# Optimization experiments

Hardware: AMD Instinct MI355X
Metric: run time of the kernel (lower is better)

The kernel has to match this reference:

```python
import jax, jax.numpy as jnp
import numpy as np

N, D_IN, H, D_EMB = 2048, 128, 256, 64


def setup_inputs() -> dict:
    key = jax.random.key(0)
    ks = jax.random.split(key, 8)
    x = jax.random.normal(ks[0], (N, D_IN), dtype=jnp.float32)
    adj = jnp.zeros((N, N), dtype=jnp.float32)  # only its last dim is used (eye sizing)
    s = 0.05
    W0 = jax.random.normal(ks[1], (D_IN, H), dtype=jnp.float32) * s
    b0 = jnp.zeros((H,), dtype=jnp.float32)
    W1 = jax.random.normal(ks[2], (H, D_EMB), dtype=jnp.float32) * s
    b1 = jnp.zeros((D_EMB,), dtype=jnp.float32)
    W2 = jax.random.normal(ks[3], (D_IN, D_IN), dtype=jnp.float32) * s
    b2 = jnp.zeros((D_IN,), dtype=jnp.float32)
    temp = jnp.float32(0.1)
    theta = jnp.float32(0.1)
    return {"x": x, "adj": adj, "W0": W0, "b0": b0, "W1": W1, "b1": b1,
            "W2": W2, "b2": b2, "temp": temp, "theta": theta}


def reference(x, adj, W0, b0, W1, b1, W2, b2, temp, theta):
    # layer 0 (on x) and middle layer 1 (on out_x), both with ReLU activation
    out_x = jax.nn.relu(x @ W0 + b0)            # [N, H]
    emb = jax.nn.relu(out_x @ W1 + b1)          # [N, D_EMB]
    # last layer is applied to the ORIGINAL x (per the `x = model(x)` branch)
    x_last = x @ W2 + b2                        # [N, D_IN]

    # dist[i,j] = -||emb_i - emb_j||^2, computed via the gemm expansion
    sq = jnp.sum(emb * emb, axis=1)             # [N]
    dist = -(sq[:, None] + sq[None, :] - 2.0 * (emb @ emb.T))  # [N, N]

    prob = jax.nn.sigmoid((1.0 + temp) * dist + (5.0 + theta))
    A = prob + jnp.eye(adj.shape[-1], dtype=prob.dtype)        # [N, N]

    # diag(A.sum(-1))^{-1} @ A @ x_last  ==  rowwise divide by degree
    deg = jnp.sum(A, axis=-1)                   # [N]
    out = jax.nn.relu((A @ x_last) / deg[:, None])

    # sigmoid(.) > 0 everywhere, so all N*N entries are nonzero: adj_wts is the
    # full flattened adjacency (data-independent shape, jit-safe)
    adj_wts = A.reshape(-1)
    return out, adj_wts
```

## Files before the change

kernel.cpp:

```cpp
#include <hip/hip_runtime.h>
#include <hip/hip_bf16.h>


typedef short bf16x8 __attribute__((ext_vector_type(8)));
typedef float f32x4 __attribute__((ext_vector_type(4)));

__device__ __forceinline__ unsigned short f2bf(float f) {
    unsigned u = __float_as_uint(f);
    unsigned r = u + 0x7fffu + ((u >> 16) & 1u);
    return (unsigned short)(r >> 16);
}

__device__ __forceinline__ bf16x8 pack_rne8(const float* p) {
    union { unsigned u[4]; bf16x8 v; } r;
    #pragma unroll
    for (int i = 0; i < 4; ++i) {
        unsigned lo = __float_as_uint(p[2 * i]) + 0x8000u;
        unsigned hi = __float_as_uint(p[2 * i + 1]) + 0x8000u;
        r.u[i] = __builtin_amdgcn_perm(hi, lo, 0x07060302u);
    }
    return r.v;
}

__device__ __forceinline__ bf16x8 pack_bf8(const float* p) {
    union { unsigned u[4]; bf16x8 v; } r;
    #pragma unroll
    for (int i = 0; i < 4; ++i)
        r.u[i] = __builtin_amdgcn_perm(__float_as_uint(p[2 * i + 1]),
                                       __float_as_uint(p[2 * i]), 0x07060302u);
    return r.v;
}

__global__ __launch_bounds__(512, 2) void k1_mfma(
    const float* __restrict__ x,
    const float* __restrict__ W0, const float* __restrict__ b0,
    const float* __restrict__ W1, const float* __restrict__ b1,
    const float* __restrict__ W2, const float* __restrict__ b2,
    unsigned short* __restrict__ emb_bf,
    unsigned short* __restrict__ xlT_bf,
    float* __restrict__ sq)
{
    constexpr int LDO = 264;
    __shared__ unsigned short oxb[16 * LDO];
    __shared__ float sqs[4][16];

    const int t = threadIdx.x;
    const int lane = t & 63;
    const int w = t >> 6;
    const int m = lane & 15;
    const int q = lane >> 4;
    const int i0 = blockIdx.x * 16;

    bf16x8 ax[4];
    #pragma unroll
    for (int kb = 0; kb < 4; ++kb) {
        float xf[8];
        *(f32x4*)&xf[0] = *(const f32x4*)(x + (size_t)(i0 + m) * 128 + kb * 32 + q * 8);
        *(f32x4*)&xf[4] = *(const f32x4*)(x + (size_t)(i0 + m) * 128 + kb * 32 + q * 8 + 4);
        ax[kb] = pack_rne8(xf);
    }

    bf16x8 wp[8];
    float bias2 = 0.f;
    if (w < 4) {
        const int h = w * 16 + m;
        bias2 = b1[h];
        #pragma unroll
        for (int kb = 0; kb < 8; ++kb) {
            float wf[8];
            #pragma unroll
            for (int j = 0; j < 8; ++j) wf[j] = W1[(size_t)(kb * 32 + q * 8 + j) * 64 + h];
            wp[kb] = pack_rne8(wf);
        }
    } else {
        const int w2 = w - 4;
        #pragma unroll
        for (int hh = 0; hh < 2; ++hh) {
            const int c = (w2 * 2 + hh) * 16 + m;
            #pragma unroll
            for (int kb = 0; kb < 4; ++kb) {
                float wf[8];
                #pragma unroll
                for (int j = 0; j < 8; ++j) wf[j] = W2[(size_t)(kb * 32 + q * 8 + j) * 128 + c];
                wp[hh * 4 + kb] = pack_rne8(wf);
            }
        }
    }

    #pragma unroll
    for (int hh = 0; hh < 2; ++hh) {
        const int h = (w * 2 + hh) * 16 + m;
        float bb = b0[h];
        f32x4 acc = {bb, bb, bb, bb};
        #pragma unroll
        for (int kb = 0; kb < 4; ++kb) {
            float wf[8];
            #pragma unroll
            for (int j = 0; j < 8; ++j) wf[j] = W0[(size_t)(kb * 32 + q * 8 + j) * 256 + h];
            acc = __builtin_amdgcn_mfma_f32_16x16x32_bf16(ax[kb], pack_rne8(wf), acc, 0, 0, 0);
        }
        #pragma unroll
        for (int r = 0; r < 4; ++r)
            oxb[(q * 4 + r) * LDO + h] = f2bf(fmaxf(acc[r], 0.0f));
    }
    __syncthreads();

    if (w < 4) {
        const int h = w * 16 + m;
        f32x4 acc = {bias2, bias2, bias2, bias2};
        #pragma unroll
        for (int kb = 0; kb < 8; ++kb) {
            bf16x8 af = *(const bf16x8*)(&oxb[m * LDO + kb * 32 + q * 8]);
            acc = __builtin_amdgcn_mfma_f32_16x16x32_bf16(af, wp[kb], acc, 0, 0, 0);
        }
        float s2[4];
        #pragma unroll
        for (int r = 0; r < 4; ++r) {
            float e = fmaxf(acc[r], 0.0f);
            emb_bf[(size_t)(i0 + q * 4 + r) * 64 + h] = f2bf(e);
            s2[r] = e * e;
        }
        #pragma unroll
        for (int r = 0; r < 4; ++r) {
            float v = s2[r];
            v += __shfl_xor(v, 1);
            v += __shfl_xor(v, 2);
            v += __shfl_xor(v, 4);
            v += __shfl_xor(v, 8);
            if (m == 0) sqs[w][q * 4 + r] = v;
        }
    } else {
        const int w2 = w - 4;
        #pragma unroll
        for (int hh = 0; hh < 2; ++hh) {
            const int c = (w2 * 2 + hh) * 16 + m;
            float bb = b2[c];
            f32x4 acc = {bb, bb, bb, bb};
            #pragma unroll
            for (int kb = 0; kb < 4; ++kb)
                acc = __builtin_amdgcn_mfma_f32_16x16x32_bf16(ax[kb], wp[hh * 4 + kb], acc, 0, 0, 0);
            uint2 pk;
            pk.x = (unsigned)f2bf(acc[0]) | ((unsigned)f2bf(acc[1]) << 16);
            pk.y = (unsigned)f2bf(acc[2]) | ((unsigned)f2bf(acc[3]) << 16);
            *(uint2*)(&xlT_bf[(size_t)c * 2048 + i0 + q * 4]) = pk;
        }
    }
    __syncthreads();
    if (t < 16)
        sq[i0 + t] = sqs[0][t] + sqs[1][t] + sqs[2][t] + sqs[3][t];
}

__global__ __launch_bounds__(256, 2) void k2f(
    const unsigned short* __restrict__ emb_bf,
    const unsigned short* __restrict__ xlT_bf,
    const float* __restrict__ sq,
    const float* __restrict__ tempp, const float* __restrict__ thetap,
    float* __restrict__ adjw,
    float* __restrict__ outPart,
    float* __restrict__ degPart)
{
    constexpr int LDP = 132;
    __shared__ float Pt[2][16 * LDP];
    __shared__ float degS[4][16];

    const int t = threadIdx.x;
    const int lane = t & 63;
    const int w = t >> 6;
    const int m = lane & 15;
    const int q = lane >> 4;
    const int i0 = blockIdx.x * 16;
    const int bj = blockIdx.y;
    const int jstrip0 = bj * 256;
    const float scale = 1.0f + tempp[0];
    const float bias = 5.0f + thetap[0];

    bf16x8 a0 = *(const bf16x8*)(emb_bf + (size_t)(i0 + m) * 64 + q * 8);
    bf16x8 a1 = *(const bf16x8*)(emb_bf + (size_t)(i0 + m) * 64 + 32 + q * 8);
    float sqIr[4];
    #pragma unroll
    for (int r = 0; r < 4; ++r) sqIr[r] = sq[i0 + q * 4 + r];

    f32x4 accO0 = {0.f, 0.f, 0.f, 0.f};
    f32x4 accO1 = {0.f, 0.f, 0.f, 0.f};
    float dega[4] = {0.f, 0.f, 0.f, 0.f};
    const int cg = w * 32;

    #pragma unroll
    for (int jt = 0; jt < 2; ++jt) {
        const int j0 = jstrip0 + jt * 128;
        float* P = &Pt[jt][0];

        bf16x8 xb[8];
        #pragma unroll
        for (int s = 0; s < 4; ++s) {
            const int k = j0 + s * 32 + q * 8;
            xb[2 * s]     = *(const bf16x8*)(xlT_bf + (size_t)(cg + m) * 2048 + k);
            xb[2 * s + 1] = *(const bf16x8*)(xlT_bf + (size_t)(cg + 16 + m) * 2048 + k);
        }

        #pragma unroll
        for (int s = 0; s < 2; ++s) {
            const int col = (w * 2 + s) * 16 + m;
            const unsigned short* ebj = emb_bf + (size_t)(j0 + col) * 64;
            bf16x8 b0 = *(const bf16x8*)(ebj + q * 8);
            bf16x8 b1 = *(const bf16x8*)(ebj + 32 + q * 8);
            f32x4 S = {0.f, 0.f, 0.f, 0.f};
            S = __builtin_amdgcn_mfma_f32_16x16x32_bf16(a0, b0, S, 0, 0, 0);
            S = __builtin_amdgcn_mfma_f32_16x16x32_bf16(a1, b1, S, 0, 0, 0);

            const float csqJ = sq[j0 + col];
            const int gcol = j0 + col;
            #pragma unroll
            for (int r = 0; r < 4; ++r) {
                int grow = i0 + q * 4 + r;
                float dist = 2.0f * S[r] - sqIr[r] - csqJ;
                float z = scale * dist + bias;
                float p = __builtin_amdgcn_rcpf(1.0f + __expf(-z));
                if (grow == gcol) p += 1.0f;
                dega[r] += p;
                P[(q * 4 + r) * LDP + col] = p;
            }
        }
        __syncthreads();

        {
            int row = t >> 5;
            int c0 = (t & 31) * 4;
            f32x4 v0 = *(const f32x4*)(&P[row * LDP + c0]);
            f32x4 v1 = *(const f32x4*)(&P[(row + 8) * LDP + c0]);
            *(f32x4*)(adjw + (size_t)(i0 + row) * 2048 + j0 + c0) = v0;
            *(f32x4*)(adjw + (size_t)(i0 + row + 8) * 2048 + j0 + c0) = v1;
        }

        #pragma unroll
        for (int s = 0; s < 4; ++s) {
            float af[8];
            *(f32x4*)(&af[0]) = *(const f32x4*)(&P[m * LDP + s * 32 + q * 8]);
            *(f32x4*)(&af[4]) = *(const f32x4*)(&P[m * LDP + s * 32 + q * 8 + 4]);
            bf16x8 aa = pack_bf8(af);
            accO0 = __builtin_amdgcn_mfma_f32_16x16x32_bf16(aa, xb[2 * s], accO0, 0, 0, 0);
            accO1 = __builtin_amdgcn_mfma_f32_16x16x32_bf16(aa, xb[2 * s + 1], accO1, 0, 0, 0);
        }
    }

    #pragma unroll
    for (int r = 0; r < 4; ++r) {
        float v = dega[r];
        v += __shfl_xor(v, 1);
        v += __shfl_xor(v, 2);
        v += __shfl_xor(v, 4);
        v += __shfl_xor(v, 8);
        if (m == 0) degS[w][q * 4 + r] = v;
    }
    __syncthreads();
    if (t < 16)
        degPart[bj * 2048 + i0 + t] =
            degS[0][t] + degS[1][t] + degS[2][t] + degS[3][t];

    float2* opf2 = (float2*)outPart + ((size_t)bj * 128 + blockIdx.x) * 1024;
    #pragma unroll
    for (int r = 0; r < 4; ++r) {
        float2 pk;
        pk.x = accO0[r];
        pk.y = accO1[r];
        opf2[((q * 4 + r) * 4 + w) * 16 + m] = pk;
    }
}

__global__ __launch_bounds__(256) void k3_fin(
    const float* __restrict__ outPart, const float* __restrict__ degPart,
    float* __restrict__ out)
{
    int gid = blockIdx.x * 256 + threadIdx.x;
    int i = gid >> 6;
    int wm = gid & 63;
    int w = wm >> 4, m = wm & 15;
    int tile = i >> 4, rit = i & 15;
    size_t base = (size_t)tile * 2048 + (size_t)((rit * 4 + w) * 16 + m) * 2;
    float s0 = 0.f, s1 = 0.f, d = 0.f;
    #pragma unroll
    for (int p = 0; p < 8; ++p) {
        const float* src = outPart + (size_t)p * 262144 + base;
        s0 += src[0];
        s1 += src[1];
        d += degPart[p * 2048 + i];
    }
    float dinv = 1.0f / d;
    out[(size_t)i * 128 + w * 32 + m] = fmaxf(s0 * dinv, 0.f);
    out[(size_t)i * 128 + w * 32 + 16 + m] = fmaxf(s1 * dinv, 0.f);
}

extern "C" void kernel_launch(void* const* d_in, const int* in_sizes, int n_in,
                              void* d_out, int out_size, void* d_ws, size_t ws_size,
                              hipStream_t stream) {
    const float* x     = (const float*)d_in[0];
    const float* W0    = (const float*)d_in[2];
    const float* b0    = (const float*)d_in[3];
    const float* W1    = (const float*)d_in[4];
    const float* b1    = (const float*)d_in[5];
    const float* W2    = (const float*)d_in[6];
    const float* b2    = (const float*)d_in[7];
    const float* temp  = (const float*)d_in[8];
    const float* theta = (const float*)d_in[9];

    char* ws = (char*)d_ws;
    unsigned short* emb_bf = (unsigned short*)(ws);
    unsigned short* xlT_bf = (unsigned short*)(ws + 262144);
    float* sq      = (float*)(ws + 786432);
    float* degPart = (float*)(ws + 794624);
    float* outPart = (float*)(ws + 860160);

    float* out  = (float*)d_out;
    float* adjw = (float*)d_out + 262144;

    k1_mfma<<<128, 512, 0, stream>>>(x, W0, b0, W1, b1, W2, b2,
                                     emb_bf, xlT_bf, sq);
    k2f<<<dim3(128, 8), 256, 0, stream>>>(emb_bf, xlT_bf, sq, temp, theta,
                                          adjw, outPart, degPart);
    k3_fin<<<512, 256, 0, stream>>>(outPart, degPart, out);
}
```

Measured before the change: 109.8 us.

## Fuse final reduction into k2 via last-block counter and split k1 roles

The first kernel is split so each 16-row tile is handled by two 256-thread blocks, one computing the two-layer MLP embedding and one the x@W2 projection, doubling block count for more parallelism. The third finalize kernel is folded into k2: each block atomically increments a per-tile counter (reset by k1) and the last of the 8 column-strip blocks reduces the partial outputs and degrees and writes the normalized result. This removes one kernel launch and its dependency gap at the cost of a threadfence plus atomic per block and a serialized tail reduction in the last block. Fusion is only enabled when the workspace is large enough for the counters.

```diff
diff --git a/kernel.cpp b/kernel.cpp
--- a/kernel.cpp
+++ b/kernel.cpp
@@ -31,14 +31,15 @@
     return r.v;
 }
 
-__global__ __launch_bounds__(512, 2) void k1_mfma(
+__global__ __launch_bounds__(256, 2) void k1_mfma(
     const float* __restrict__ x,
     const float* __restrict__ W0, const float* __restrict__ b0,
     const float* __restrict__ W1, const float* __restrict__ b1,
     const float* __restrict__ W2, const float* __restrict__ b2,
     unsigned short* __restrict__ emb_bf,
     unsigned short* __restrict__ xlT_bf,
-    float* __restrict__ sq)
+    float* __restrict__ sq,
+    int* __restrict__ cnt)
 {
     constexpr int LDO = 264;
     __shared__ unsigned short oxb[16 * LDO];
@@ -49,7 +50,11 @@
     const int w = t >> 6;
     const int m = lane & 15;
     const int q = lane >> 4;
-    const int i0 = blockIdx.x * 16;
+    const int tile = blockIdx.x >> 1;
+    const int role = blockIdx.x & 1;
+    const int i0 = tile * 16;
+
+    if (cnt && role && t == 0) cnt[tile] = 0;
 
     bf16x8 ax[4];
     #pragma unroll
@@ -60,54 +65,37 @@
         ax[kb] = pack_rne8(xf);
     }
 
-    bf16x8 wp[8];
-    float bias2 = 0.f;
-    if (w < 4) {
-        const int h = w * 16 + m;
-        bias2 = b1[h];
+    if (role == 0) {
+        const int h1 = w * 16 + m;
+        const float bias1 = b1[h1];
+        bf16x8 wp[8];
         #pragma unroll
         for (int kb = 0; kb < 8; ++kb) {
             float wf[8];
             #pragma unroll
-            for (int j = 0; j < 8; ++j) wf[j] = W1[(size_t)(kb * 32 + q * 8 + j) * 64 + h];
+            for (int j = 0; j < 8; ++j) wf[j] = W1[(size_t)(kb * 32 + q * 8 + j) * 64 + h1];
             wp[kb] = pack_rne8(wf);
         }
-    } else {
-        const int w2 = w - 4;
-        #pragma unroll
-        for (int hh = 0; hh < 2; ++hh) {
-            const int c = (w2 * 2 + hh) * 16 + m;
+
+        #pragma unroll
+        for (int hh = 0; hh < 4; ++hh) {
+            const int h = (w * 4 + hh) * 16 + m;
+            float bb = b0[h];
+            f32x4 acc = {bb, bb, bb, bb};
             #pragma unroll
             for (int kb = 0; kb < 4; ++kb) {
                 float wf[8];
                 #pragma unroll
-                for (int j = 0; j < 8; ++j) wf[j] = W2[(size_t)(kb * 32 + q * 8 + j) * 128 + c];
-                wp[hh * 4 + kb] = pack_rne8(wf);
+                for (int j = 0; j < 8; ++j) wf[j] = W0[(size_t)(kb * 32 + q * 8 + j) * 256 + h];
+                acc = __builtin_amdgcn_mfma_f32_16x16x32_bf16(ax[kb], pack_rne8(wf), acc, 0, 0, 0);
             }
-        }
-    }
-
-    #pragma unroll
-    for (int hh = 0; hh < 2; ++hh) {
-        const int h = (w * 2 + hh) * 16 + m;
-        float bb = b0[h];
-        f32x4 acc = {bb, bb, bb, bb};
-        #pragma unroll
-        for (int kb = 0; kb < 4; ++kb) {
-            float wf[8];
-            #pragma unroll
-            for (int j = 0; j < 8; ++j) wf[j] = W0[(size_t)(kb * 32 + q * 8 + j) * 256 + h];
-            acc = __builtin_amdgcn_mfma_f32_16x16x32_bf16(ax[kb], pack_rne8(wf), acc, 0, 0, 0);
-        }
-        #pragma unroll
-        for (int r = 0; r < 4; ++r)
-            oxb[(q * 4 + r) * LDO + h] = f2bf(fmaxf(acc[r], 0.0f));
-    }
-    __syncthreads();
-
-    if (w < 4) {
-        const int h = w * 16 + m;
-        f32x4 acc = {bias2, bias2, bias2, bias2};
+            #pragma unroll
+            for (int r = 0; r < 4; ++r)
+                oxb[(q * 4 + r) * LDO + h] = f2bf(fmaxf(acc[r], 0.0f));
+        }
+        __syncthreads();
+
+        f32x4 acc = {bias1, bias1, bias1, bias1};
         #pragma unroll
         for (int kb = 0; kb < 8; ++kb) {
             bf16x8 af = *(const bf16x8*)(&oxb[m * LDO + kb * 32 + q * 8]);
@@ -117,7 +105,7 @@
         #pragma unroll
         for (int r = 0; r < 4; ++r) {
             float e = fmaxf(acc[r], 0.0f);
-            emb_bf[(size_t)(i0 + q * 4 + r) * 64 + h] = f2bf(e);
+            emb_bf[(size_t)(i0 + q * 4 + r) * 64 + h1] = f2bf(e);
             s2[r] = e * e;
         }
         #pragma unroll
@@ -129,11 +117,25 @@
             v += __shfl_xor(v, 8);
             if (m == 0) sqs[w][q * 4 + r] = v;
         }
+        __syncthreads();
+        if (t < 16)
+            sq[i0 + t] = sqs[0][t] + sqs[1][t] + sqs[2][t] + sqs[3][t];
     } else {
-        const int w2 = w - 4;
+        bf16x8 wp[8];
         #pragma unroll
         for (int hh = 0; hh < 2; ++hh) {
-            const int c = (w2 * 2 + hh) * 16 + m;
+            const int c = (w * 2 + hh) * 16 + m;
+            #pragma unroll
+            for (int kb = 0; kb < 4; ++kb) {
+                float wf[8];
+                #pragma unroll
+                for (int j = 0; j < 8; ++j) wf[j] = W2[(size_t)(kb * 32 + q * 8 + j) * 128 + c];
+                wp[hh * 4 + kb] = pack_rne8(wf);
+            }
+        }
+        #pragma unroll
+        for (int hh = 0; hh < 2; ++hh) {
+            const int c = (w * 2 + hh) * 16 + m;
             float bb = b2[c];
             f32x4 acc = {bb, bb, bb, bb};
             #pragma unroll
@@ -145,9 +147,6 @@
             *(uint2*)(&xlT_bf[(size_t)c * 2048 + i0 + q * 4]) = pk;
         }
     }
-    __syncthreads();
-    if (t < 16)
-        sq[i0 + t] = sqs[0][t] + sqs[1][t] + sqs[2][t] + sqs[3][t];
 }
 
 __global__ __launch_bounds__(256, 2) void k2f(
@@ -157,11 +156,14 @@
     const float* __restrict__ tempp, const float* __restrict__ thetap,
     float* __restrict__ adjw,
     float* __restrict__ outPart,
-    float* __restrict__ degPart)
+    float* __restrict__ degPart,
+    float* __restrict__ out,
+    int* __restrict__ cnt)
 {
     constexpr int LDP = 132;
     __shared__ float Pt[2][16 * LDP];
     __shared__ float degS[4][16];
+    __shared__ int lastFlag;
 
     const int t = threadIdx.x;
     const int lane = t & 63;
@@ -264,6 +266,38 @@
         pk.x = accO0[r];
         pk.y = accO1[r];
         opf2[((q * 4 + r) * 4 + w) * 16 + m] = pk;
+    }
+
+    if (cnt == nullptr) return;
+
+    __threadfence();
+    __syncthreads();
+    if (t == 0)
+        lastFlag = (atomicAdd(&cnt[blockIdx.x], 1) == 7);
+    __syncthreads();
+    if (lastFlag) {
+        __threadfence();
+        const int tile = blockIdx.x;
+        #pragma unroll
+        for (int it = 0; it < 4; ++it) {
+            const int idx = it * 256 + t;
+            const int rit = idx >> 6;
+            const int w3 = (idx >> 4) & 3;
+            const int m3 = idx & 15;
+            const int i = tile * 16 + rit;
+            const size_t base = (size_t)tile * 2048 + (size_t)idx * 2;
+            float s0 = 0.f, s1 = 0.f, d = 0.f;
+            #pragma unroll
+            for (int p = 0; p < 8; ++p) {
+                const float* src = outPart + (size_t)p * 262144 + base;
+                s0 += src[0];
+                s1 += src[1];
+                d += degPart[p * 2048 + i];
+            }
+            float dinv = 1.0f / d;
+            out[(size_t)i * 128 + w3 * 32 + m3]      = fmaxf(s0 * dinv, 0.f);
+            out[(size_t)i * 128 + w3 * 32 + 16 + m3] = fmaxf(s1 * dinv, 0.f);
+        }
     }
 }
 
@@ -293,6 +327,7 @@
 extern "C" void kernel_launch(void* const* d_in, const int* in_sizes, int n_in,
                               void* d_out, int out_size, void* d_ws, size_t ws_size,
                               hipStream_t stream) {
+    (void)in_sizes; (void)n_in; (void)out_size;
     const float* x     = (const float*)d_in[0];
     const float* W0    = (const float*)d_in[2];
     const float* b0    = (const float*)d_in[3];
@@ -309,13 +344,16 @@
     float* sq      = (float*)(ws + 786432);
     float* degPart = (float*)(ws + 794624);
     float* outPart = (float*)(ws + 860160);
+    const bool fused = (ws_size >= 9248768 + 512);
+    int* cnt = fused ? (int*)(ws + 9248768) : nullptr;
 
     float* out  = (float*)d_out;
     float* adjw = (float*)d_out + 262144;
 
-    k1_mfma<<<128, 512, 0, stream>>>(x, W0, b0, W1, b1, W2, b2,
-                                     emb_bf, xlT_bf, sq);
+    k1_mfma<<<256, 256, 0, stream>>>(x, W0, b0, W1, b1, W2, b2,
+                                     emb_bf, xlT_bf, sq, cnt);
     k2f<<<dim3(128, 8), 256, 0, stream>>>(emb_bf, xlT_bf, sq, temp, theta,
-                                          adjw, outPart, degPart);
-    k3_fin<<<512, 256, 0, stream>>>(outPart, degPart, out);
-}
+                                          adjw, outPart, degPart, out, cnt);
+    if (!fused)
+        k3_fin<<<512, 256, 0, stream>>>(outPart, degPart, out);
+}
```

Result: slower. 232.4 us (+111.7%).

## Pre-transpose weights to bf16 and split MLP and last-layer into separate blocks

Applied to the files above, without the earlier changes.

Adds a prep kernel that transposes and converts W0, W1 and W2 to bf16, so the MLP kernel loads each weight fragment as one 16-byte vector instead of eight strided fp32 loads. The first kernel is also split into two block roles per 16-row tile: one computes the two-layer MLP with emb and sq, the other computes x@W2. This doubles the grid at 256 threads per block. The cost is an extra kernel launch and an extra workspace region; if the workspace is too small, the old strided-load path is used.

```diff
diff --git a/kernel.cpp b/kernel.cpp
--- a/kernel.cpp
+++ b/kernel.cpp
@@ -11,6 +11,10 @@
     return (unsigned short)(r >> 16);
 }
 
+__device__ __forceinline__ unsigned short f2bf_hu(float f) {
+    return (unsigned short)((__float_as_uint(f) + 0x8000u) >> 16);
+}
+
 __device__ __forceinline__ bf16x8 pack_rne8(const float* p) {
     union { unsigned u[4]; bf16x8 v; } r;
     #pragma unroll
@@ -31,11 +35,37 @@
     return r.v;
 }
 
-__global__ __launch_bounds__(512, 2) void k1_mfma(
+__global__ __launch_bounds__(256) void k0_prep(
+    const float* __restrict__ W0, const float* __restrict__ W1,
+    const float* __restrict__ W2,
+    unsigned short* __restrict__ W0T,
+    unsigned short* __restrict__ W1T,
+    unsigned short* __restrict__ W2T)
+{
+    const int gid = blockIdx.x * 256 + threadIdx.x;
+    {
+        const int h = gid >> 7, k = gid & 127;
+        W0T[gid] = f2bf_hu(W0[(size_t)k * 256 + h]);
+    }
+    if (gid < 16384) {
+        const int h = gid >> 8, k = gid & 255;
+        W1T[gid] = f2bf_hu(W1[(size_t)k * 64 + h]);
+    } else {
+        const int o = gid - 16384;
+        const int c = o >> 7, k = o & 127;
+        W2T[o] = f2bf_hu(W2[(size_t)k * 128 + c]);
+    }
+}
+
+template<int VEC>
+__global__ __launch_bounds__(256, 2) void k1_mfma(
     const float* __restrict__ x,
     const float* __restrict__ W0, const float* __restrict__ b0,
     const float* __restrict__ W1, const float* __restrict__ b1,
     const float* __restrict__ W2, const float* __restrict__ b2,
+    const unsigned short* __restrict__ W0T,
+    const unsigned short* __restrict__ W1T,
+    const unsigned short* __restrict__ W2T,
     unsigned short* __restrict__ emb_bf,
     unsigned short* __restrict__ xlT_bf,
     float* __restrict__ sq)
@@ -49,7 +79,9 @@
     const int w = t >> 6;
     const int m = lane & 15;
     const int q = lane >> 4;
-    const int i0 = blockIdx.x * 16;
+    const int tile = blockIdx.x >> 1;
+    const int role = blockIdx.x & 1;
+    const int i0 = tile * 16;
 
     bf16x8 ax[4];
     #pragma unroll
@@ -60,54 +92,47 @@
         ax[kb] = pack_rne8(xf);
     }
 
-    bf16x8 wp[8];
-    float bias2 = 0.f;
-    if (w < 4) {
-        const int h = w * 16 + m;
-        bias2 = b1[h];
+    if (role == 0) {
+        const int h1 = w * 16 + m;
+        const float bias1 = b1[h1];
+        bf16x8 wp[8];
         #pragma unroll
         for (int kb = 0; kb < 8; ++kb) {
-            float wf[8];
-            #pragma unroll
-            for (int j = 0; j < 8; ++j) wf[j] = W1[(size_t)(kb * 32 + q * 8 + j) * 64 + h];
-            wp[kb] = pack_rne8(wf);
-        }
-    } else {
-        const int w2 = w - 4;
-        #pragma unroll
-        for (int hh = 0; hh < 2; ++hh) {
-            const int c = (w2 * 2 + hh) * 16 + m;
-            #pragma unroll
-            for (int kb = 0; kb < 4; ++kb) {
+            if (VEC) {
+                wp[kb] = *(const bf16x8*)(W1T + (size_t)h1 * 256 + kb * 32 + q * 8);
+            } else {
                 float wf[8];
                 #pragma unroll
-                for (int j = 0; j < 8; ++j) wf[j] = W2[(size_t)(kb * 32 + q * 8 + j) * 128 + c];
-                wp[hh * 4 + kb] = pack_rne8(wf);
+                for (int j = 0; j < 8; ++j) wf[j] = W1[(size_t)(kb * 32 + q * 8 + j) * 64 + h1];
+                wp[kb] = pack_rne8(wf);
             }
         }
-    }
-
-    #pragma unroll
-    for (int hh = 0; hh < 2; ++hh) {
-        const int h = (w * 2 + hh) * 16 + m;
-        float bb = b0[h];
-        f32x4 acc = {bb, bb, bb, bb};
-        #pragma unroll
-        for (int kb = 0; kb < 4; ++kb) {
-            float wf[8];
-            #pragma unroll
-            for (int j = 0; j < 8; ++j) wf[j] = W0[(size_t)(kb * 32 + q * 8 + j) * 256 + h];
-            acc = __builtin_amdgcn_mfma_f32_16x16x32_bf16(ax[kb], pack_rne8(wf), acc, 0, 0, 0);
-        }
-        #pragma unroll
-        for (int r = 0; r < 4; ++r)
-            oxb[(q * 4 + r) * LDO + h] = f2bf(fmaxf(acc[r], 0.0f));
-    }
-    __syncthreads();
-
-    if (w < 4) {
-        const int h = w * 16 + m;
-        f32x4 acc = {bias2, bias2, bias2, bias2};
+
+        #pragma unroll
+        for (int hh = 0; hh < 4; ++hh) {
+            const int h = (w * 4 + hh) * 16 + m;
+            float bb = b0[h];
+            f32x4 acc = {bb, bb, bb, bb};
+            #pragma unroll
+            for (int kb = 0; kb < 4; ++kb) {
+                bf16x8 bfrag;
+                if (VEC) {
+                    bfrag = *(const bf16x8*)(W0T + (size_t)h * 128 + kb * 32 + q * 8);
+                } else {
+                    float wf[8];
+                    #pragma unroll
+                    for (int j = 0; j < 8; ++j) wf[j] = W0[(size_t)(kb * 32 + q * 8 + j) * 256 + h];
+                    bfrag = pack_rne8(wf);
+                }
+                acc = __builtin_amdgcn_mfma_f32_16x16x32_bf16(ax[kb], bfrag, acc, 0, 0, 0);
+            }
+            #pragma unroll
+            for (int r = 0; r < 4; ++r)
+                oxb[(q * 4 + r) * LDO + h] = f2bf(fmaxf(acc[r], 0.0f));
+        }
+        __syncthreads();
+
+        f32x4 acc = {bias1, bias1, bias1, bias1};
         #pragma unroll
         for (int kb = 0; kb < 8; ++kb) {
             bf16x8 af = *(const bf16x8*)(&oxb[m * LDO + kb * 32 + q * 8]);
@@ -117,7 +142,7 @@
         #pragma unroll
         for (int r = 0; r < 4; ++r) {
             float e = fmaxf(acc[r], 0.0f);
-            emb_bf[(size_t)(i0 + q * 4 + r) * 64 + h] = f2bf(e);
+            emb_bf[(size_t)(i0 + q * 4 + r) * 64 + h1] = f2bf(e);
             s2[r] = e * e;
         }
         #pragma unroll
@@ -129,11 +154,29 @@
             v += __shfl_xor(v, 8);
             if (m == 0) sqs[w][q * 4 + r] = v;
         }
+        __syncthreads();
+        if (t < 16)
+            sq[i0 + t] = sqs[0][t] + sqs[1][t] + sqs[2][t] + sqs[3][t];
     } else {
-        const int w2 = w - 4;
+        bf16x8 wp[8];
         #pragma unroll
         for (int hh = 0; hh < 2; ++hh) {
-            const int c = (w2 * 2 + hh) * 16 + m;
+            const int c = (w * 2 + hh) * 16 + m;
+            #pragma unroll
+            for (int kb = 0; kb < 4; ++kb) {
+                if (VEC) {
+                    wp[hh * 4 + kb] = *(const bf16x8*)(W2T + (size_t)c * 128 + kb * 32 + q * 8);
+                } else {
+                    float wf[8];
+                    #pragma unroll
+                    for (int j = 0; j < 8; ++j) wf[j] = W2[(size_t)(kb * 32 + q * 8 + j) * 128 + c];
+                    wp[hh * 4 + kb] = pack_rne8(wf);
+                }
+            }
+        }
+        #pragma unroll
+        for (int hh = 0; hh < 2; ++hh) {
+            const int c = (w * 2 + hh) * 16 + m;
             float bb = b2[c];
             f32x4 acc = {bb, bb, bb, bb};
             #pragma unroll
@@ -145,9 +188,6 @@
             *(uint2*)(&xlT_bf[(size_t)c * 2048 + i0 + q * 4]) = pk;
         }
     }
-    __syncthreads();
-    if (t < 16)
-        sq[i0 + t] = sqs[0][t] + sqs[1][t] + sqs[2][t] + sqs[3][t];
 }
 
 __global__ __launch_bounds__(256, 2) void k2f(
@@ -293,6 +333,7 @@
 extern "C" void kernel_launch(void* const* d_in, const int* in_sizes, int n_in,
                               void* d_out, int out_size, void* d_ws, size_t ws_size,
                               hipStream_t stream) {
+    (void)in_sizes; (void)n_in; (void)out_size;
     const float* x     = (const float*)d_in[0];
     const float* W0    = (const float*)d_in[2];
     const float* b0    = (const float*)d_in[3];
@@ -309,12 +350,22 @@
     float* sq      = (float*)(ws + 786432);
     float* degPart = (float*)(ws + 794624);
     float* outPart = (float*)(ws + 860160);
+    unsigned short* W0T = (unsigned short*)(ws + 9248768);
+    unsigned short* W1T = (unsigned short*)(ws + 9314304);
+    unsigned short* W2T = (unsigned short*)(ws + 9347072);
+    const bool vec = (ws_size >= 9379840);
 
     float* out  = (float*)d_out;
     float* adjw = (float*)d_out + 262144;
 
-    k1_mfma<<<128, 512, 0, stream>>>(x, W0, b0, W1, b1, W2, b2,
-                                     emb_bf, xlT_bf, sq);
+    if (vec) {
+        k0_prep<<<128, 256, 0, stream>>>(W0, W1, W2, W0T, W1T, W2T);
+        k1_mfma<1><<<256, 256, 0, stream>>>(x, W0, b0, W1, b1, W2, b2,
+                                            W0T, W1T, W2T, emb_bf, xlT_bf, sq);
+    } else {
+        k1_mfma<0><<<256, 256, 0, stream>>>(x, W0, b0, W1, b1, W2, b2,
+                                            W0T, W1T, W2T, emb_bf, xlT_bf, sq);
+    }
     k2f<<<dim3(128, 8), 256, 0, stream>>>(emb_bf, xlT_bf, sq, temp, theta,
                                           adjw, outPart, degPart);
     k3_fin<<<512, 256, 0, stream>>>(outPart, degPart, out);
```

Result: no change. 108.9 us (-0.8%).

## Split k1 into role blocks and rebalance k2 into fewer, larger j-halves

Applied to the files above, without the earlier changes.

k1 now runs twice as many 256-thread blocks, each dedicated to either the MLP-embedding path or the x@W2 path, instead of splitting warps within one block. k2 uses 512-thread blocks covering half the j range each (8 strips of 128 looped), with each warp owning 16 output columns, so there are only 2 partial sums instead of 8. k3 becomes a simple vectorized two-way reduction. This cuts partial-output traffic and reduction work, but k2 now launches 256 blocks, which may underfill the GPU, and each block runs a longer serial loop.

```diff
diff --git a/kernel.cpp b/kernel.cpp
--- a/kernel.cpp
+++ b/kernel.cpp
@@ -31,7 +31,7 @@
     return r.v;
 }
 
-__global__ __launch_bounds__(512, 2) void k1_mfma(
+__global__ __launch_bounds__(256, 2) void k1_mfma(
     const float* __restrict__ x,
     const float* __restrict__ W0, const float* __restrict__ b0,
     const float* __restrict__ W1, const float* __restrict__ b1,
@@ -49,7 +49,9 @@
     const int w = t >> 6;
     const int m = lane & 15;
     const int q = lane >> 4;
-    const int i0 = blockIdx.x * 16;
+    const int tile = blockIdx.x >> 1;
+    const int role = blockIdx.x & 1;
+    const int i0 = tile * 16;
 
     bf16x8 ax[4];
     #pragma unroll
@@ -60,54 +62,37 @@
         ax[kb] = pack_rne8(xf);
     }
 
-    bf16x8 wp[8];
-    float bias2 = 0.f;
-    if (w < 4) {
-        const int h = w * 16 + m;
-        bias2 = b1[h];
+    if (role == 0) {
+        const int h1 = w * 16 + m;
+        const float bias1 = b1[h1];
+        bf16x8 wp[8];
         #pragma unroll
         for (int kb = 0; kb < 8; ++kb) {
             float wf[8];
             #pragma unroll
-            for (int j = 0; j < 8; ++j) wf[j] = W1[(size_t)(kb * 32 + q * 8 + j) * 64 + h];
+            for (int j = 0; j < 8; ++j) wf[j] = W1[(size_t)(kb * 32 + q * 8 + j) * 64 + h1];
             wp[kb] = pack_rne8(wf);
         }
-    } else {
-        const int w2 = w - 4;
-        #pragma unroll
-        for (int hh = 0; hh < 2; ++hh) {
-            const int c = (w2 * 2 + hh) * 16 + m;
+
+        #pragma unroll
+        for (int hh = 0; hh < 4; ++hh) {
+            const int h = (w * 4 + hh) * 16 + m;
+            float bb = b0[h];
+            f32x4 acc = {bb, bb, bb, bb};
             #pragma unroll
             for (int kb = 0; kb < 4; ++kb) {
                 float wf[8];
                 #pragma unroll
-                for (int j = 0; j < 8; ++j) wf[j] = W2[(size_t)(kb * 32 + q * 8 + j) * 128 + c];
-                wp[hh * 4 + kb] = pack_rne8(wf);
+                for (int j = 0; j < 8; ++j) wf[j] = W0[(size_t)(kb * 32 + q * 8 + j) * 256 + h];
+                acc = __builtin_amdgcn_mfma_f32_16x16x32_bf16(ax[kb], pack_rne8(wf), acc, 0, 0, 0);
             }
-        }
-    }
-
-    #pragma unroll
-    for (int hh = 0; hh < 2; ++hh) {
-        const int h = (w * 2 + hh) * 16 + m;
-        float bb = b0[h];
-        f32x4 acc = {bb, bb, bb, bb};
-        #pragma unroll
-        for (int kb = 0; kb < 4; ++kb) {
-            float wf[8];
-            #pragma unroll
-            for (int j = 0; j < 8; ++j) wf[j] = W0[(size_t)(kb * 32 + q * 8 + j) * 256 + h];
-            acc = __builtin_amdgcn_mfma_f32_16x16x32_bf16(ax[kb], pack_rne8(wf), acc, 0, 0, 0);
-        }
-        #pragma unroll
-        for (int r = 0; r < 4; ++r)
-            oxb[(q * 4 + r) * LDO + h] = f2bf(fmaxf(acc[r], 0.0f));
-    }
-    __syncthreads();
-
-    if (w < 4) {
-        const int h = w * 16 + m;
-        f32x4 acc = {bias2, bias2, bias2, bias2};
+            #pragma unroll
+            for (int r = 0; r < 4; ++r)
+                oxb[(q * 4 + r) * LDO + h] = f2bf(fmaxf(acc[r], 0.0f));
+        }
+        __syncthreads();
+
+        f32x4 acc = {bias1, bias1, bias1, bias1};
         #pragma unroll
         for (int kb = 0; kb < 8; ++kb) {
             bf16x8 af = *(const bf16x8*)(&oxb[m * LDO + kb * 32 + q * 8]);
@@ -117,7 +102,7 @@
         #pragma unroll
         for (int r = 0; r < 4; ++r) {
             float e = fmaxf(acc[r], 0.0f);
-            emb_bf[(size_t)(i0 + q * 4 + r) * 64 + h] = f2bf(e);
+            emb_bf[(size_t)(i0 + q * 4 + r) * 64 + h1] = f2bf(e);
             s2[r] = e * e;
         }
         #pragma unroll
@@ -129,11 +114,25 @@
             v += __shfl_xor(v, 8);
             if (m == 0) sqs[w][q * 4 + r] = v;
         }
+        __syncthreads();
+        if (t < 16)
+            sq[i0 + t] = sqs[0][t] + sqs[1][t] + sqs[2][t] + sqs[3][t];
     } else {
-        const int w2 = w - 4;
+        bf16x8 wp[8];
         #pragma unroll
         for (int hh = 0; hh < 2; ++hh) {
-            const int c = (w2 * 2 + hh) * 16 + m;
+            const int c = (w * 2 + hh) * 16 + m;
+            #pragma unroll
+            for (int kb = 0; kb < 4; ++kb) {
+                float wf[8];
+                #pragma unroll
+                for (int j = 0; j < 8; ++j) wf[j] = W2[(size_t)(kb * 32 + q * 8 + j) * 128 + c];
+                wp[hh * 4 + kb] = pack_rne8(wf);
+            }
+        }
+        #pragma unroll
+        for (int hh = 0; hh < 2; ++hh) {
+            const int c = (w * 2 + hh) * 16 + m;
             float bb = b2[c];
             f32x4 acc = {bb, bb, bb, bb};
             #pragma unroll
@@ -145,12 +144,9 @@
             *(uint2*)(&xlT_bf[(size_t)c * 2048 + i0 + q * 4]) = pk;
         }
     }
-    __syncthreads();
-    if (t < 16)
-        sq[i0 + t] = sqs[0][t] + sqs[1][t] + sqs[2][t] + sqs[3][t];
-}
-
-__global__ __launch_bounds__(256, 2) void k2f(
+}
+
+__global__ __launch_bounds__(512, 4) void k2h(
     const unsigned short* __restrict__ emb_bf,
     const unsigned short* __restrict__ xlT_bf,
     const float* __restrict__ sq,
@@ -161,7 +157,7 @@
 {
     constexpr int LDP = 132;
     __shared__ float Pt[2][16 * LDP];
-    __shared__ float degS[4][16];
+    __shared__ float degS[8][16];
 
     const int t = threadIdx.x;
     const int lane = t & 63;
@@ -169,8 +165,8 @@
     const int m = lane & 15;
     const int q = lane >> 4;
     const int i0 = blockIdx.x * 16;
-    const int bj = blockIdx.y;
-    const int jstrip0 = bj * 256;
+    const int half = blockIdx.y;
+    const int jbase = half * 1024;
     const float scale = 1.0f + tempp[0];
     const float bias = 5.0f + thetap[0];
 
@@ -180,36 +176,30 @@
     #pragma unroll
     for (int r = 0; r < 4; ++r) sqIr[r] = sq[i0 + q * 4 + r];
 
-    f32x4 accO0 = {0.f, 0.f, 0.f, 0.f};
-    f32x4 accO1 = {0.f, 0.f, 0.f, 0.f};
+    f32x4 accO = {0.f, 0.f, 0.f, 0.f};
     float dega[4] = {0.f, 0.f, 0.f, 0.f};
-    const int cg = w * 32;
-
-    #pragma unroll
-    for (int jt = 0; jt < 2; ++jt) {
-        const int j0 = jstrip0 + jt * 128;
-        float* P = &Pt[jt][0];
-
-        bf16x8 xb[8];
-        #pragma unroll
-        for (int s = 0; s < 4; ++s) {
-            const int k = j0 + s * 32 + q * 8;
-            xb[2 * s]     = *(const bf16x8*)(xlT_bf + (size_t)(cg + m) * 2048 + k);
-            xb[2 * s + 1] = *(const bf16x8*)(xlT_bf + (size_t)(cg + 16 + m) * 2048 + k);
-        }
-
-        #pragma unroll
-        for (int s = 0; s < 2; ++s) {
-            const int col = (w * 2 + s) * 16 + m;
-            const unsigned short* ebj = emb_bf + (size_t)(j0 + col) * 64;
+    const int cg = w * 16;
+
+    for (int jt = 0; jt < 8; ++jt) {
+        const int j0 = jbase + jt * 128;
+        float* P = &Pt[jt & 1][0];
+
+        bf16x8 xb[4];
+        #pragma unroll
+        for (int s = 0; s < 4; ++s)
+            xb[s] = *(const bf16x8*)(xlT_bf + (size_t)(cg + m) * 2048 + j0 + s * 32 + q * 8);
+
+        {
+            const int col = w * 16 + m;
+            const int gcol = j0 + col;
+            const unsigned short* ebj = emb_bf + (size_t)gcol * 64;
             bf16x8 b0 = *(const bf16x8*)(ebj + q * 8);
             bf16x8 b1 = *(const bf16x8*)(ebj + 32 + q * 8);
             f32x4 S = {0.f, 0.f, 0.f, 0.f};
             S = __builtin_amdgcn_mfma_f32_16x16x32_bf16(a0, b0, S, 0, 0, 0);
             S = __builtin_amdgcn_mfma_f32_16x16x32_bf16(a1, b1, S, 0, 0, 0);
 
-            const float csqJ = sq[j0 + col];
-            const int gcol = j0 + col;
+            const float csqJ = sq[gcol];
             #pragma unroll
             for (int r = 0; r < 4; ++r) {
                 int grow = i0 + q * 4 + r;
@@ -226,10 +216,8 @@
         {
             int row = t >> 5;
             int c0 = (t & 31) * 4;
-            f32x4 v0 = *(const f32x4*)(&P[row * LDP + c0]);
-            f32x4 v1 = *(const f32x4*)(&P[(row + 8) * LDP + c0]);
-            *(f32x4*)(adjw + (size_t)(i0 + row) * 2048 + j0 + c0) = v0;
-            *(f32x4*)(adjw + (size_t)(i0 + row + 8) * 2048 + j0 + c0) = v1;
+            f32x4 v = *(const f32x4*)(&P[row * LDP + c0]);
+            *(f32x4*)(adjw + (size_t)(i0 + row) * 2048 + j0 + c0) = v;
         }
 
         #pragma unroll
@@ -238,8 +226,7 @@
             *(f32x4*)(&af[0]) = *(const f32x4*)(&P[m * LDP + s * 32 + q * 8]);
             *(f32x4*)(&af[4]) = *(const f32x4*)(&P[m * LDP + s * 32 + q * 8 + 4]);
             bf16x8 aa = pack_bf8(af);
-            accO0 = __builtin_amdgcn_mfma_f32_16x16x32_bf16(aa, xb[2 * s], accO0, 0, 0, 0);
-            accO1 = __builtin_amdgcn_mfma_f32_16x16x32_bf16(aa, xb[2 * s + 1], accO1, 0, 0, 0);
+            accO = __builtin_amdgcn_mfma_f32_16x16x32_bf16(aa, xb[s], accO, 0, 0, 0);
         }
     }
 
@@ -253,18 +240,17 @@
         if (m == 0) degS[w][q * 4 + r] = v;
     }
     __syncthreads();
-    if (t < 16)
-        degPart[bj * 2048 + i0 + t] =
-            degS[0][t] + degS[1][t] + degS[2][t] + degS[3][t];
-
-    float2* opf2 = (float2*)outPart + ((size_t)bj * 128 + blockIdx.x) * 1024;
-    #pragma unroll
-    for (int r = 0; r < 4; ++r) {
-        float2 pk;
-        pk.x = accO0[r];
-        pk.y = accO1[r];
-        opf2[((q * 4 + r) * 4 + w) * 16 + m] = pk;
-    }
+    if (t < 16) {
+        float d = 0.f;
+        #pragma unroll
+        for (int ww = 0; ww < 8; ++ww) d += degS[ww][t];
+        degPart[half * 2048 + i0 + t] = d;
+    }
+
+    float* op = outPart + (size_t)half * 262144 + (size_t)i0 * 128 + cg + m;
+    #pragma unroll
+    for (int r = 0; r < 4; ++r)
+        op[(size_t)(q * 4 + r) * 128] = accO[r];
 }
 
 __global__ __launch_bounds__(256) void k3_fin(
@@ -272,27 +258,21 @@
     float* __restrict__ out)
 {
     int gid = blockIdx.x * 256 + threadIdx.x;
-    int i = gid >> 6;
-    int wm = gid & 63;
-    int w = wm >> 4, m = wm & 15;
-    int tile = i >> 4, rit = i & 15;
-    size_t base = (size_t)tile * 2048 + (size_t)((rit * 4 + w) * 16 + m) * 2;
-    float s0 = 0.f, s1 = 0.f, d = 0.f;
-    #pragma unroll
-    for (int p = 0; p < 8; ++p) {
-        const float* src = outPart + (size_t)p * 262144 + base;
-        s0 += src[0];
-        s1 += src[1];
-        d += degPart[p * 2048 + i];
-    }
-    float dinv = 1.0f / d;
-    out[(size_t)i * 128 + w * 32 + m] = fmaxf(s0 * dinv, 0.f);
-    out[(size_t)i * 128 + w * 32 + 16 + m] = fmaxf(s1 * dinv, 0.f);
+    int i = gid >> 5;
+    int c0 = (gid & 31) * 4;
+    f32x4 v0 = *(const f32x4*)(outPart + (size_t)i * 128 + c0);
+    f32x4 v1 = *(const f32x4*)(outPart + 262144 + (size_t)i * 128 + c0);
+    float dinv = 1.0f / (degPart[i] + degPart[2048 + i]);
+    f32x4 o;
+    #pragma unroll
+    for (int r = 0; r < 4; ++r) o[r] = fmaxf((v0[r] + v1[r]) * dinv, 0.f);
+    *(f32x4*)(out + (size_t)i * 128 + c0) = o;
 }
 
 extern "C" void kernel_launch(void* const* d_in, const int* in_sizes, int n_in,
                               void* d_out, int out_size, void* d_ws, size_t ws_size,
                               hipStream_t stream) {
+    (void)in_sizes; (void)n_in; (void)out_size; (void)ws_size;
     const float* x     = (const float*)d_in[0];
     const float* W0    = (const float*)d_in[2];
     const float* b0    = (const float*)d_in[3];
@@ -308,14 +288,14 @@
     unsigned short* xlT_bf = (unsigned short*)(ws + 262144);
     float* sq      = (float*)(ws + 786432);
     float* degPart = (float*)(ws + 794624);
-    float* outPart = (float*)(ws + 860160);
+    float* outPart = (float*)(ws + 811008);
 
     float* out  = (float*)d_out;
     float* adjw = (float*)d_out + 262144;
 
-    k1_mfma<<<128, 512, 0, stream>>>(x, W0, b0, W1, b1, W2, b2,
+    k1_mfma<<<256, 256, 0, stream>>>(x, W0, b0, W1, b1, W2, b2,
                                      emb_bf, xlT_bf, sq);
-    k2f<<<dim3(128, 8), 256, 0, stream>>>(emb_bf, xlT_bf, sq, temp, theta,
+    k2h<<<dim3(128, 2), 512, 0, stream>>>(emb_bf, xlT_bf, sq, temp, theta,
                                           adjw, outPart, degPart);
-    k3_fin<<<512, 256, 0, stream>>>(outPart, degPart, out);
-}
+    k3_fin<<<256, 256, 0, stream>>>(outPart, degPart, out);
+}
```

Measured after the change: 108.0 us, median of 2. Within noise of the previous version (-1.6%).
